# Kernel tuning notes

Measured on AMD Instinct MI355X. Metric: run time of the kernel, lower is better.

The kernel has to match this reference:

```python
import jax, jax.numpy as jnp
import numpy as np

B, L, H, W, C = 2, 5, 48, 48, 256
M, D = 8, 32               # heads, dim_head; M*D == C
NT, NR = 2, 4              # num_types, num_relations
SCALE = D ** -0.5
EPS = 1e-5


def _xavier(k, shape):
    fan_out, fan_in = shape[-2], shape[-1]
    lim = (6.0 / (fan_in + fan_out)) ** 0.5
    return jax.random.uniform(k, shape, jnp.float32, -lim, lim)


def setup_inputs() -> dict:
    key = jax.random.key(0)
    ks = jax.random.split(key, 10)
    inner = M * D
    x = jax.random.normal(ks[0], (B, L, H, W, C), jnp.float32)
    mask = jnp.ones((B, H, W, L, L), jnp.int32)
    pe = jax.random.randint(ks[1], (B, L, H, W, 3), 0, NT).astype(jnp.float32)
    return dict(
        x=x, mask=mask, prior_encoding=pe,
        ln_w=jnp.ones((C,), jnp.float32), ln_b=jnp.zeros((C,), jnp.float32),
        q_weight=_xavier(ks[2], (NT, inner, C)), q_bias=jnp.zeros((NT, inner), jnp.float32),
        k_weight=_xavier(ks[3], (NT, inner, C)), k_bias=jnp.zeros((NT, inner), jnp.float32),
        v_weight=_xavier(ks[4], (NT, inner, C)), v_bias=jnp.zeros((NT, inner), jnp.float32),
        a_weight=_xavier(ks[5], (NT, C, inner)), a_bias=jnp.zeros((NT, C), jnp.float32),
        relation_att=_xavier(ks[6], (NR, M, D, D)),
        relation_msg=_xavier(ks[7], (NR, M, D, D)),
    )


def reference(x, mask, prior_encoding, ln_w, ln_b,
              q_weight, q_bias, k_weight, k_bias, v_weight, v_bias,
              a_weight, a_bias, relation_att, relation_msg):
    # PreNorm (torch LayerNorm: biased variance, eps=1e-5)
    mu = jnp.mean(x, axis=-1, keepdims=True)
    var = jnp.mean((x - mu) ** 2, axis=-1, keepdims=True)
    xn = (x - mu) * jax.lax.rsqrt(var + EPS) * ln_w + ln_b

    types = prior_encoding[:, :, 0, 0, 2].astype(jnp.int32)  # (B, L)
    xp = jnp.transpose(xn, (0, 2, 3, 1, 4))                  # (B, H, W, L, C)

    def type_linear(inp, wgt, b):
        # gather per-node-type weights (B,L,out,in) and project
        return (jnp.einsum('bhwlc,bloc->bhwlo', inp, wgt[types])
                + b[types][:, None, None, :, :])

    def to_heads(t):
        # (B,H,W,L,M*D) -> (B,M,H,W,L,D)
        return jnp.transpose(t.reshape(B, H, W, L, M, D), (0, 4, 1, 2, 3, 5))

    q = to_heads(type_linear(xp, q_weight, q_bias))
    k = to_heads(type_linear(xp, k_weight, k_bias))
    v = to_heads(type_linear(xp, v_weight, v_bias))

    # per-edge relation weights: rel_idx = t_i * num_types + t_j
    rel = types[:, :, None] * NT + types[:, None, :]          # (B, L, L)
    w_att = jnp.transpose(relation_att[rel], (0, 3, 1, 2, 4, 5))  # (B,M,L,L,D,D)
    w_msg = jnp.transpose(relation_msg[rel], (0, 3, 1, 2, 4, 5))  # (B,M,L,L,D,D)

    q_w = jnp.einsum('bmhwip,bmijpq->bmhwijq', q, w_att)
    att = jnp.einsum('bmhwijq,bmhwjq->bmhwij', q_w, k) * SCALE
    att = jnp.where(mask[:, None] == 0, -1e9, att)
    att = jax.nn.softmax(att, axis=-1)

    v_msg = jnp.einsum('bmijpc,bmhwjp->bmhwijc', w_msg, v)
    out = jnp.einsum('bmhwij,bmhwijc->bmhwic', att, v_msg)
    out = jnp.transpose(out, (0, 2, 3, 4, 1, 5)).reshape(B, H, W, L, C)

    # output projection with per-type weights (dropout = identity at eval)
    out = (jnp.einsum('bhwli,blci->bhwlc', out, a_weight[types])
           + a_bias[types][:, None, None, :, :])
    return jnp.transpose(out, (0, 3, 1, 2, 4))  # (B, L, H, W, C)
```

## Files before the change

kernel.cpp:

```cpp
#include <hip/hip_runtime.h>
#include <hip/hip_bf16.h>

#define BB 2
#define LL 5
#define HH 48
#define WW 48
#define CC 256
#define MM 8
#define DD 32
#define HWW (HH*WW)
#define NTOK (BB*LL*HWW)
#define INNER 256
#define NOUT 1280
#define SCALE_ATT 0.17677669529663687f

typedef __hip_bfloat16 bf16;
typedef short short8 __attribute__((ext_vector_type(8)));
typedef short short4v __attribute__((ext_vector_type(4)));
typedef float f32x4  __attribute__((ext_vector_type(4)));

__device__ __forceinline__ float b2f(bf16 v){ return __bfloat162float(v); }
__device__ __forceinline__ bf16 f2b(float v){ return __float2bfloat16(v); }
__device__ __forceinline__ short f2s(float v){
  bf16 h = __float2bfloat16(v);
  return *reinterpret_cast<short*>(&h);
}

__global__ __launch_bounds__(256) void ln_fused_kernel(
    const float* __restrict__ x, const float* __restrict__ lnw,
    const float* __restrict__ lnb, bf16* __restrict__ xn)
{
  int tok  = blockIdx.x*4 + (threadIdx.x>>6);
  int lane = threadIdx.x & 63;
  const float4* xr = (const float4*)(x + (size_t)tok*CC);
  float4 v = xr[lane];
  float s  = v.x + v.y + v.z + v.w;
  float sq = v.x*v.x + v.y*v.y + v.z*v.z + v.w*v.w;
  #pragma unroll
  for(int off=32; off>=1; off>>=1){
    s  += __shfl_xor(s,  off, 64);
    sq += __shfl_xor(sq, off, 64);
  }
  float m   = s  * (1.f/CC);
  float var = sq * (1.f/CC) - m*m;
  float rs  = rsqrtf(var + 1e-5f);
  float4 w = *(const float4*)(lnw + lane*4);
  float4 c = *(const float4*)(lnb + lane*4);
  short4v pk;
  pk[0] = f2s((v.x-m)*rs*w.x + c.x);
  pk[1] = f2s((v.y-m)*rs*w.y + c.y);
  pk[2] = f2s((v.z-m)*rs*w.z + c.z);
  pk[3] = f2s((v.w-m)*rs*w.w + c.w);
  *reinterpret_cast<short4v*>(xn + (size_t)tok*CC + lane*4) = pk;
}

__global__ __launch_bounds__(256) void wcomp_kernel(
    const float* __restrict__ qw, const float* __restrict__ qb,
    const float* __restrict__ kw, const float* __restrict__ kb,
    const float* __restrict__ vw, const float* __restrict__ vb,
    const float* __restrict__ ra, const float* __restrict__ rm,
    bf16* __restrict__ W_all, float* __restrict__ b_all)
{
  int bid = blockIdx.x;
  int t = bid / 320, nb = bid % 320;
  int tid = threadIdx.x;
  int wv = tid>>6, lane = tid&63;
  int n = nb*4 + wv;

  float a0=0.f,a1=0.f,a2=0.f,a3=0.f, bias=0.f;
  if(n < 512 || n >= 768){
    bool isq = (n < 512);
    int nr = isq ? n : n-768;
    int s = nr>>8, mdp = nr&255, m = mdp>>5, dp = mdp&31;
    int r = isq ? (2*t+s) : (2*s+t);
    const float* rel  = (isq ? ra : rm) + ((size_t)r*MM + m)*DD*DD + dp;
    const float* wrow = (isq ? qw : vw) + (size_t)t*INNER*CC + (size_t)m*DD*CC;
    const float* brow = (isq ? qb : vb) + t*INNER + m*DD;
    #pragma unroll
    for(int p=0;p<DD;p++){
      float rv = rel[p*DD];
      float4 w4 = *(const float4*)(wrow + p*CC + lane*4);
      a0 += w4.x*rv; a1 += w4.y*rv; a2 += w4.z*rv; a3 += w4.w*rv;
      bias += brow[p]*rv;
    }
  } else {
    int o = n - 512;
    float4 w4 = *(const float4*)(kw + (size_t)t*INNER*CC + (size_t)o*CC + lane*4);
    a0=w4.x; a1=w4.y; a2=w4.z; a3=w4.w;
    bias = kb[t*INNER + o];
  }
  bf16* dst = W_all + ((size_t)t*NOUT + n)*CC + lane*4;
  dst[0]=f2b(a0); dst[1]=f2b(a1); dst[2]=f2b(a2); dst[3]=f2b(a3);
  if(lane==0) b_all[t*NOUT + n] = bias;
}

__global__ __launch_bounds__(256) void qkvm_gemm_kernel(
    const bf16* __restrict__ xn,  const float* __restrict__ pe,
    const bf16* __restrict__ W_all, const float* __restrict__ b_all,
    bf16* __restrict__ qkvm)
{
  int g = blockIdx.z;
  int t = (int)pe[(size_t)g*HWW*3 + 2];
  int o_base = blockIdx.x * 128;
  const bf16*  wsel = W_all + ((size_t)t*NOUT + o_base)*CC;
  const float* bsel = b_all + t*NOUT;
  int row_base = blockIdx.y*128;
  int tid = threadIdx.x;
  int tokbase = g*HWW + row_base;

  __shared__ __align__(16) short A_s[128*64];
  __shared__ __align__(16) short B_s[128*64];

  int wv = tid>>6, lane = tid&63;
  int wr = wv>>1, wc = wv&1;
  int l16 = lane&15, l4 = lane>>4;
  int kc = tid & 7;
  int rsub = tid >> 3;

  f32x4 acc[4][4];
  #pragma unroll
  for(int i=0;i<4;i++)
    #pragma unroll
    for(int j=0;j<4;j++) acc[i][j] = (f32x4){0.f,0.f,0.f,0.f};

  for(int kk=0; kk<CC; kk+=64){
    if(kk) __syncthreads();
    #pragma unroll
    for(int tt=0; tt<4; tt++){
      int row = rsub + tt*32;
      short8 pk = *reinterpret_cast<const short8*>(
          xn + (size_t)(tokbase + row)*CC + kk + kc*8);
      int el = (row*64 + kc*8) ^ ((row&7)<<3);
      *reinterpret_cast<short8*>(&A_s[el]) = pk;
    }
    #pragma unroll
    for(int tt=0; tt<4; tt++){
      int n = rsub + tt*32;
      short8 pk = *reinterpret_cast<const short8*>(wsel + (size_t)n*CC + kk + kc*8);
      int el = (n*64 + kc*8) ^ ((n&7)<<3);
      *reinterpret_cast<short8*>(&B_s[el]) = pk;
    }
    __syncthreads();
    #pragma unroll
    for(int ks=0; ks<2; ks++){
      short8 af[4], bfr[4];
      #pragma unroll
      for(int fr=0; fr<4; fr++){
        int row = wr*64 + fr*16 + l16;
        int el = (row*64 + ks*32 + l4*8) ^ ((row&7)<<3);
        af[fr] = *reinterpret_cast<const short8*>(&A_s[el]);
      }
      #pragma unroll
      for(int fc=0; fc<4; fc++){
        int n = wc*64 + fc*16 + l16;
        int el = (n*64 + ks*32 + l4*8) ^ ((n&7)<<3);
        bfr[fc] = *reinterpret_cast<const short8*>(&B_s[el]);
      }
      #pragma unroll
      for(int fr=0; fr<4; fr++)
        #pragma unroll
        for(int fc=0; fc<4; fc++)
          acc[fr][fc] = __builtin_amdgcn_mfma_f32_16x16x32_bf16(af[fr], bfr[fc], acc[fr][fc], 0,0,0);
    }
  }
  #pragma unroll
  for(int fr=0; fr<4; fr++){
    #pragma unroll
    for(int fc=0; fc<4; fc++){
      int ocol = o_base + wc*64 + fc*16 + l16;
      float bias = bsel[ocol];
      #pragma unroll
      for(int r=0; r<4; r++){
        int row = row_base + wr*64 + fr*16 + l4*4 + r;
        qkvm[((size_t)g*HWW + row)*NOUT + ocol] = f2b(acc[fr][fc][r] + bias);
      }
    }
  }
}

__global__ __launch_bounds__(256) void attn_lite_kernel(
    const bf16* __restrict__ qkvm, const float* __restrict__ pe,
    const int*  __restrict__ mask, bf16* __restrict__ attn_out)
{
  int pix = blockIdx.x;
  int b = pix / HWW, hw = pix - b*HWW;
  int tid = threadIdx.x;
  int m = tid>>5, d = tid&31;

  __shared__ int st[LL];
  __shared__ unsigned mbS;
  if(tid==0) mbS = 0u;
  if(tid<LL) st[tid] = (int)pe[(size_t)(b*LL+tid)*HWW*3 + 2];
  __syncthreads();
  const int* mrow = mask + ((size_t)b*HWW + hw)*25;
  if(tid<25 && mrow[tid]==0) atomicOr(&mbS, 1u<<tid);
  __syncthreads();
  unsigned mb = mbS;

  float qa[LL][2], kv[LL], vm[LL][2];
  #pragma unroll
  for(int l=0;l<LL;l++){
    size_t base = ((size_t)(b*LL+l)*HWW + hw)*NOUT + m*DD + d;
    qa[l][0] = b2f(qkvm[base]);
    qa[l][1] = b2f(qkvm[base+256]);
    kv[l]    = b2f(qkvm[base+512]);
    vm[l][0] = b2f(qkvm[base+768]);
    vm[l][1] = b2f(qkvm[base+1024]);
  }

  float p[LL][LL];
  #pragma unroll
  for(int i=0;i<LL;i++){
    #pragma unroll
    for(int j=0;j<LL;j++){
      int stj = st[j];
      float part = (stj ? qa[i][1] : qa[i][0]) * kv[j];
      #pragma unroll
      for(int off=16; off>=1; off>>=1) part += __shfl_xor(part, off, 32);
      p[i][j] = (mb & (1u<<(i*5+j))) ? -1e9f : part*SCALE_ATT;
    }
  }
  #pragma unroll
  for(int i=0;i<LL;i++){
    float mx = p[i][0];
    #pragma unroll
    for(int j=1;j<LL;j++) mx = fmaxf(mx, p[i][j]);
    float ssum = 0.f;
    #pragma unroll
    for(int j=0;j<LL;j++){ p[i][j] = __expf(p[i][j]-mx); ssum += p[i][j]; }
    float inv = 1.f/ssum;
    int sti = st[i];
    float o = 0.f;
    #pragma unroll
    for(int j=0;j<LL;j++) o += p[i][j] * (sti ? vm[j][1] : vm[j][0]);
    o *= inv;
    attn_out[(((size_t)b*HWW + hw)*LL + i)*CC + m*DD + d] = f2b(o);
  }
}

__global__ __launch_bounds__(256) void out_gemm_kernel(
    const bf16* __restrict__ attn_out, const float* __restrict__ pe,
    const float* __restrict__ aw, const float* __restrict__ ab,
    float* __restrict__ out)
{
  int g = blockIdx.z; int b = g/LL, l = g%LL;
  int t = (int)pe[(size_t)g*HWW*3 + 2];
  int o_base = blockIdx.x*128;
  int row_base = blockIdx.y*128;
  int tid = threadIdx.x;
  const float* wsel = aw + ((size_t)t*CC + o_base)*CC;

  __shared__ __align__(16) short A_s[128*64];
  __shared__ __align__(16) short B_s[128*64];

  int wv = tid>>6, lane = tid&63;
  int wr = wv>>1, wc = wv&1;
  int l16 = lane&15, l4 = lane>>4;
  int kc = tid & 7;
  int rsub = tid >> 3;

  f32x4 acc[4][4];
  #pragma unroll
  for(int i=0;i<4;i++)
    #pragma unroll
    for(int j=0;j<4;j++) acc[i][j] = (f32x4){0.f,0.f,0.f,0.f};

  for(int kk=0; kk<CC; kk+=64){
    if(kk) __syncthreads();
    #pragma unroll
    for(int tt=0; tt<4; tt++){
      int row = rsub + tt*32;
      short8 pk = *reinterpret_cast<const short8*>(
          attn_out + (((size_t)(b*HWW) + row_base + row)*LL + l)*CC + kk + kc*8);
      int el = (row*64 + kc*8) ^ ((row&7)<<3);
      *reinterpret_cast<short8*>(&A_s[el]) = pk;
    }
    #pragma unroll
    for(int tt=0; tt<4; tt++){
      int n = rsub + tt*32;
      const float4* src = (const float4*)(wsel + (size_t)n*CC + kk + kc*8);
      float4 ba = src[0], bb = src[1];
      short8 pk;
      pk[0]=f2s(ba.x); pk[1]=f2s(ba.y); pk[2]=f2s(ba.z); pk[3]=f2s(ba.w);
      pk[4]=f2s(bb.x); pk[5]=f2s(bb.y); pk[6]=f2s(bb.z); pk[7]=f2s(bb.w);
      int el = (n*64 + kc*8) ^ ((n&7)<<3);
      *reinterpret_cast<short8*>(&B_s[el]) = pk;
    }
    __syncthreads();
    #pragma unroll
    for(int ks=0; ks<2; ks++){
      short8 af[4], bfr[4];
      #pragma unroll
      for(int fr=0; fr<4; fr++){
        int row = wr*64 + fr*16 + l16;
        int el = (row*64 + ks*32 + l4*8) ^ ((row&7)<<3);
        af[fr] = *reinterpret_cast<const short8*>(&A_s[el]);
      }
      #pragma unroll
      for(int fc=0; fc<4; fc++){
        int n = wc*64 + fc*16 + l16;
        int el = (n*64 + ks*32 + l4*8) ^ ((n&7)<<3);
        bfr[fc] = *reinterpret_cast<const short8*>(&B_s[el]);
      }
      #pragma unroll
      for(int fr=0; fr<4; fr++)
        #pragma unroll
        for(int fc=0; fc<4; fc++)
          acc[fr][fc] = __builtin_amdgcn_mfma_f32_16x16x32_bf16(af[fr], bfr[fc], acc[fr][fc], 0,0,0);
    }
  }
  #pragma unroll
  for(int fr=0; fr<4; fr++){
    #pragma unroll
    for(int fc=0; fc<4; fc++){
      int ocol = o_base + wc*64 + fc*16 + l16;
      float bias = ab[t*CC + ocol];
      #pragma unroll
      for(int r=0; r<4; r++){
        int row = row_base + wr*64 + fr*16 + l4*4 + r;
        out[((size_t)g*HWW + row)*CC + ocol] = acc[fr][fc][r] + bias;
      }
    }
  }
}

extern "C" void kernel_launch(void* const* d_in, const int* in_sizes, int n_in,
                              void* d_out, int out_size, void* d_ws, size_t ws_size,
                              hipStream_t stream)
{
  const float* x   = (const float*)d_in[0];
  const int*   mask= (const int*)  d_in[1];
  const float* pe  = (const float*)d_in[2];
  const float* lnw = (const float*)d_in[3];
  const float* lnb = (const float*)d_in[4];
  const float* qw  = (const float*)d_in[5];
  const float* qb  = (const float*)d_in[6];
  const float* kw  = (const float*)d_in[7];
  const float* kb  = (const float*)d_in[8];
  const float* vw  = (const float*)d_in[9];
  const float* vb  = (const float*)d_in[10];
  const float* aw  = (const float*)d_in[11];
  const float* ab  = (const float*)d_in[12];
  const float* ra  = (const float*)d_in[13];
  const float* rm  = (const float*)d_in[14];

  char* ws = (char*)d_ws;
  bf16*  xn    = (bf16*) ws;
  bf16*  attn  = (bf16*) ws;
  bf16*  W_all = (bf16*) (ws + 11796480);
  float* b_all = (float*)(ws + 13107200);
  bf16*  qkvm  = (bf16*) (ws + 13117440);
  float* out   = (float*)d_out;

  hipLaunchKernelGGL(ln_fused_kernel, dim3(NTOK/4), dim3(256), 0, stream,
                     x, lnw, lnb, xn);
  hipLaunchKernelGGL(wcomp_kernel, dim3(640), dim3(256), 0, stream,
                     qw, qb, kw, kb, vw, vb, ra, rm, W_all, b_all);
  hipLaunchKernelGGL(qkvm_gemm_kernel, dim3(10, 18, 10), dim3(256), 0, stream,
                     xn, pe, W_all, b_all, qkvm);
  hipLaunchKernelGGL(attn_lite_kernel, dim3(BB*HWW), dim3(256), 0, stream,
                     qkvm, pe, mask, attn);
  hipLaunchKernelGGL(out_gemm_kernel, dim3(2, 18, 10), dim3(256), 0, stream,
                     attn, pe, aw, ab, out);
}
```

Before: 179.1 us.

## Load GEMM tiles straight into LDS and pre-convert output weights to bf16

Both GEMM kernels now stage their A and B tiles with global_load_lds direct-to-LDS 16-byte loads, replacing the register round trip. The XOR swizzle is kept by permuting the source column each lane fetches. The output projection weights are converted to bf16 once inside wcomp_kernel, so out_gemm no longer reads fp32 weights and converts them in every block. This cuts register pressure and VALU work in the load phase, but it relies on the direct-load LDS layout matching the existing read swizzle.

```diff
diff --git a/kernel.cpp b/kernel.cpp
--- a/kernel.cpp
+++ b/kernel.cpp
@@ -18,12 +18,18 @@
 typedef short short8 __attribute__((ext_vector_type(8)));
 typedef short short4v __attribute__((ext_vector_type(4)));
 typedef float f32x4  __attribute__((ext_vector_type(4)));
+typedef unsigned int u32;
+typedef const __attribute__((address_space(1))) u32* gp32;
+typedef __attribute__((address_space(3))) u32* lp32;
 
 __device__ __forceinline__ float b2f(bf16 v){ return __bfloat162float(v); }
 __device__ __forceinline__ bf16 f2b(float v){ return __float2bfloat16(v); }
 __device__ __forceinline__ short f2s(float v){
   bf16 h = __float2bfloat16(v);
   return *reinterpret_cast<short*>(&h);
+}
+__device__ __forceinline__ void gload16(const void* g, void* l){
+  __builtin_amdgcn_global_load_lds((gp32)g, (lp32)l, 16, 0, 0);
 }
 
 __global__ __launch_bounds__(256) void ln_fused_kernel(
@@ -59,11 +65,16 @@
     const float* __restrict__ kw, const float* __restrict__ kb,
     const float* __restrict__ vw, const float* __restrict__ vb,
     const float* __restrict__ ra, const float* __restrict__ rm,
+    const float* __restrict__ aw, bf16* __restrict__ aw_bf,
     bf16* __restrict__ W_all, float* __restrict__ b_all)
 {
   int bid = blockIdx.x;
+  int tid = threadIdx.x;
+  {
+    int idx = bid*256 + tid;
+    if(idx < 2*CC*CC) aw_bf[idx] = f2b(aw[idx]);
+  }
   int t = bid / 320, nb = bid % 320;
-  int tid = threadIdx.x;
   int wv = tid>>6, lane = tid&63;
   int n = nb*4 + wv;
 
@@ -114,8 +125,8 @@
   int wv = tid>>6, lane = tid&63;
   int wr = wv>>1, wc = wv&1;
   int l16 = lane&15, l4 = lane>>4;
-  int kc = tid & 7;
-  int rsub = tid >> 3;
+  int lr = lane>>3;
+  int sw = (lane&7) ^ lr;
 
   f32x4 acc[4][4];
   #pragma unroll
@@ -126,19 +137,11 @@
   for(int kk=0; kk<CC; kk+=64){
     if(kk) __syncthreads();
     #pragma unroll
-    for(int tt=0; tt<4; tt++){
-      int row = rsub + tt*32;
-      short8 pk = *reinterpret_cast<const short8*>(
-          xn + (size_t)(tokbase + row)*CC + kk + kc*8);
-      int el = (row*64 + kc*8) ^ ((row&7)<<3);
-      *reinterpret_cast<short8*>(&A_s[el]) = pk;
-    }
-    #pragma unroll
-    for(int tt=0; tt<4; tt++){
-      int n = rsub + tt*32;
-      short8 pk = *reinterpret_cast<const short8*>(wsel + (size_t)n*CC + kk + kc*8);
-      int el = (n*64 + kc*8) ^ ((n&7)<<3);
-      *reinterpret_cast<short8*>(&B_s[el]) = pk;
+    for(int i=0;i<4;i++){
+      int ci  = wv*4 + i;
+      int row = ci*8 + lr;
+      gload16(xn  + (size_t)(tokbase + row)*CC + kk + sw*8, &A_s[ci*512]);
+      gload16(wsel + (size_t)row*CC          + kk + sw*8, &B_s[ci*512]);
     }
     __syncthreads();
     #pragma unroll
@@ -240,7 +243,7 @@
 
 __global__ __launch_bounds__(256) void out_gemm_kernel(
     const bf16* __restrict__ attn_out, const float* __restrict__ pe,
-    const float* __restrict__ aw, const float* __restrict__ ab,
+    const bf16* __restrict__ aw_bf, const float* __restrict__ ab,
     float* __restrict__ out)
 {
   int g = blockIdx.z; int b = g/LL, l = g%LL;
@@ -248,7 +251,7 @@
   int o_base = blockIdx.x*128;
   int row_base = blockIdx.y*128;
   int tid = threadIdx.x;
-  const float* wsel = aw + ((size_t)t*CC + o_base)*CC;
+  const bf16* wsel = aw_bf + ((size_t)t*CC + o_base)*CC;
 
   __shared__ __align__(16) short A_s[128*64];
   __shared__ __align__(16) short B_s[128*64];
@@ -256,8 +259,8 @@
   int wv = tid>>6, lane = tid&63;
   int wr = wv>>1, wc = wv&1;
   int l16 = lane&15, l4 = lane>>4;
-  int kc = tid & 7;
-  int rsub = tid >> 3;
+  int lr = lane>>3;
+  int sw = (lane&7) ^ lr;
 
   f32x4 acc[4][4];
   #pragma unroll
@@ -268,23 +271,12 @@
   for(int kk=0; kk<CC; kk+=64){
     if(kk) __syncthreads();
     #pragma unroll
-    for(int tt=0; tt<4; tt++){
-      int row = rsub + tt*32;
-      short8 pk = *reinterpret_cast<const short8*>(
-          attn_out + (((size_t)(b*HWW) + row_base + row)*LL + l)*CC + kk + kc*8);
-      int el = (row*64 + kc*8) ^ ((row&7)<<3);
-      *reinterpret_cast<short8*>(&A_s[el]) = pk;
-    }
-    #pragma unroll
-    for(int tt=0; tt<4; tt++){
-      int n = rsub + tt*32;
-      const float4* src = (const float4*)(wsel + (size_t)n*CC + kk + kc*8);
-      float4 ba = src[0], bb = src[1];
-      short8 pk;
-      pk[0]=f2s(ba.x); pk[1]=f2s(ba.y); pk[2]=f2s(ba.z); pk[3]=f2s(ba.w);
-      pk[4]=f2s(bb.x); pk[5]=f2s(bb.y); pk[6]=f2s(bb.z); pk[7]=f2s(bb.w);
-      int el = (n*64 + kc*8) ^ ((n&7)<<3);
-      *reinterpret_cast<short8*>(&B_s[el]) = pk;
+    for(int i=0;i<4;i++){
+      int ci  = wv*4 + i;
+      int row = ci*8 + lr;
+      gload16(attn_out + (((size_t)(b*HWW) + row_base + row)*LL + l)*CC + kk + sw*8,
+              &A_s[ci*512]);
+      gload16(wsel + (size_t)row*CC + kk + sw*8, &B_s[ci*512]);
     }
     __syncthreads();
     #pragma unroll
@@ -350,16 +342,17 @@
   bf16*  W_all = (bf16*) (ws + 11796480);
   float* b_all = (float*)(ws + 13107200);
   bf16*  qkvm  = (bf16*) (ws + 13117440);
+  bf16*  aw_bf = (bf16*) (ws + 72099840);
   float* out   = (float*)d_out;
 
   hipLaunchKernelGGL(ln_fused_kernel, dim3(NTOK/4), dim3(256), 0, stream,
                      x, lnw, lnb, xn);
   hipLaunchKernelGGL(wcomp_kernel, dim3(640), dim3(256), 0, stream,
-                     qw, qb, kw, kb, vw, vb, ra, rm, W_all, b_all);
+                     qw, qb, kw, kb, vw, vb, ra, rm, aw, aw_bf, W_all, b_all);
   hipLaunchKernelGGL(qkvm_gemm_kernel, dim3(10, 18, 10), dim3(256), 0, stream,
                      xn, pe, W_all, b_all, qkvm);
   hipLaunchKernelGGL(attn_lite_kernel, dim3(BB*HWW), dim3(256), 0, stream,
                      qkvm, pe, mask, attn);
   hipLaunchKernelGGL(out_gemm_kernel, dim3(2, 18, 10), dim3(256), 0, stream,
-                     attn, pe, aw, ab, out);
-}
+                     attn, pe, aw_bf, ab, out);
+}
```

New measurement: 173.3 us. 3.2% less time.
